# Optimization experiments

Hardware: AMD Instinct MI355X
Metric: run time of the kernel (lower is better)

The kernel has to match this reference:

```python
import jax, jax.numpy as jnp
import numpy as np

# Model dims (mamba_ssm defaults: expand=2, d_state=16, d_conv=4, dt_rank=ceil(d_model/16))
V, D_MODEL, N_LAYERS = 32000, 768, 2
D_INNER, D_STATE, D_CONV, DT_RANK = 1536, 16, 4, 48
BATCH, SEQ = 2, 2048


def setup_inputs() -> dict:
    key = jax.random.key(0)
    ks = jax.random.split(key, 10)

    def nrm(k, shape, s=0.02):
        return (jax.random.normal(k, shape) * s).astype(jnp.float32)

    x = jax.random.randint(ks[0], (BATCH, SEQ), 0, V)
    emb = nrm(ks[1], (V, D_MODEL))
    # per-layer Mamba params, stacked on leading layer axis
    W_in = nrm(ks[2], (N_LAYERS, 2 * D_INNER, D_MODEL))          # in_proj (no bias)
    conv_w = nrm(ks[3], (N_LAYERS, D_INNER, 1, D_CONV), 0.1)      # depthwise causal conv
    conv_b = jnp.zeros((N_LAYERS, D_INNER), jnp.float32)
    W_x = nrm(ks[4], (N_LAYERS, DT_RANK + 2 * D_STATE, D_INNER))  # x_proj (no bias)
    W_dt = nrm(ks[5], (N_LAYERS, D_INNER, DT_RANK), 0.05)         # dt_proj
    b_dt = jnp.full((N_LAYERS, D_INNER), -4.0, jnp.float32)       # softplus(-4) ~ small dt
    # A initialized as -exp(A_log) with A_log = log(1..d_state), per mamba_ssm
    A_log = jnp.log(jnp.broadcast_to(
        jnp.arange(1, D_STATE + 1, dtype=jnp.float32), (N_LAYERS, D_INNER, D_STATE)))
    D_skip = jnp.ones((N_LAYERS, D_INNER), jnp.float32)
    W_out = nrm(ks[6], (N_LAYERS, D_MODEL, D_INNER))              # out_proj (no bias)
    ln_g = jnp.ones((D_MODEL,), jnp.float32)
    ln_b = jnp.zeros((D_MODEL,), jnp.float32)
    head_w = nrm(ks[7], (V, D_MODEL))
    head_b = jnp.zeros((V,), jnp.float32)
    return dict(x=x, emb=emb, W_in=W_in, conv_w=conv_w, conv_b=conv_b, W_x=W_x,
                W_dt=W_dt, b_dt=b_dt, A_log=A_log, D_skip=D_skip, W_out=W_out,
                ln_g=ln_g, ln_b=ln_b, head_w=head_w, head_b=head_b)


def mamba_block(h, W_in, conv_w, conv_b, W_x, W_dt, b_dt, A_log, D_skip, W_out):
    # h: (B, L, D_MODEL)
    xz = jnp.einsum('bld,ed->ble', h, W_in)              # (B, L, 2*d_inner)
    u, z = jnp.split(xz, 2, axis=-1)
    # causal depthwise conv over time
    uc = jnp.transpose(u, (0, 2, 1))                     # (B, d_inner, L)
    uc = jax.lax.conv_general_dilated(
        uc, conv_w, window_strides=(1,), padding=[(D_CONV - 1, 0)],
        feature_group_count=D_INNER, dimension_numbers=('NCH', 'OIH', 'NCH'))
    u = jax.nn.silu(jnp.transpose(uc, (0, 2, 1)) + conv_b)
    # input-dependent dt, B, C
    x_dbl = jnp.einsum('bld,ed->ble', u, W_x)            # (B, L, dt_rank+2*d_state)
    dtl, Bm, Cm = jnp.split(x_dbl, [DT_RANK, DT_RANK + D_STATE], axis=-1)
    dt = jax.nn.softplus(jnp.einsum('blr,dr->bld', dtl, W_dt) + b_dt)  # (B, L, d_inner)
    A = -jnp.exp(A_log)                                  # (d_inner, d_state)

    def step(hst, inp):
        dt_t, u_t, B_t, C_t = inp                        # (B,d_inner),(B,d_inner),(B,d_state),(B,d_state)
        hst = jnp.exp(dt_t[..., None] * A) * hst + (dt_t * u_t)[..., None] * B_t[:, None, :]
        y_t = jnp.einsum('bds,bs->bd', hst, C_t)
        return hst, y_t

    h0 = jnp.zeros((u.shape[0], D_INNER, D_STATE), u.dtype)
    xs = (dt.transpose(1, 0, 2), u.transpose(1, 0, 2),
          Bm.transpose(1, 0, 2), Cm.transpose(1, 0, 2))
    _, ys = jax.lax.scan(step, h0, xs)                   # (L, B, d_inner)
    y = ys.transpose(1, 0, 2) + u * D_skip
    y = y * jax.nn.silu(z)
    return jnp.einsum('bli,oi->blo', y, W_out)           # back to (B, L, D_MODEL)


def reference(x, emb, W_in, conv_w, conv_b, W_x, W_dt, b_dt, A_log, D_skip,
              W_out, ln_g, ln_b, head_w, head_b):
    h = emb[x]                                           # (B, L, D_MODEL)
    for l in range(N_LAYERS):
        h = h + mamba_block(h, W_in[l], conv_w[l], conv_b[l], W_x[l], W_dt[l],
                            b_dt[l], A_log[l], D_skip[l], W_out[l])
    mu = jnp.mean(h, axis=-1, keepdims=True)
    var = jnp.mean((h - mu) ** 2, axis=-1, keepdims=True)
    hn = (h - mu) * jax.lax.rsqrt(var + 1e-5) * ln_g + ln_b
    return jnp.einsum('bld,vd->blv', hn, head_w) + head_b
```

## Files before the change

kernel.cpp:

```cpp
#include <hip/hip_runtime.h>
#include <hip/hip_bf16.h>
#include <stdint.h>

#define BL    4096
#define DM    768
#define DI    1536
#define DS    16
#define DCONV 4
#define DTR   48
#define NL    2
#define SEQL  2048
#define BATCH 2
#define VOC   32000
#define NCH   32
#define CT    64

typedef __bf16 bf16_t;
typedef __bf16 bf16x8 __attribute__((ext_vector_type(8)));
typedef __bf16 bf16x4 __attribute__((ext_vector_type(4)));
typedef float  f32x4  __attribute__((ext_vector_type(4)));

__device__ __forceinline__ float sigmoidf_(float x) { return 1.f / (1.f + __expf(-x)); }
__device__ __forceinline__ float softplus_(float x) {
  return (x > 20.f) ? x : log1pf(__expf(x));
}

__global__ __launch_bounds__(256) void k_embed(const int* __restrict__ x,
                                               const float* __restrict__ emb,
                                               float* __restrict__ h,
                                               bf16_t* __restrict__ hb) {
  int row = blockIdx.x;
  int tok = x[row];
  const float* e = emb + (size_t)tok * DM;
  float* hr = h + (size_t)row * DM;
  bf16_t* hbr = hb + (size_t)row * DM;
  for (int c = threadIdx.x; c < DM; c += 256) {
    float v = e[c];
    hr[c] = v;
    hbr[c] = (bf16_t)v;
  }
}

#define NV0 1179648L
#define NV1 589824L
#define NV2 6144000L
#define NS3 393216L
#define NS4 196608L
#define NVT (NV0 + NV1 + NV2)
#define NTOT (NVT + NS3 + NS4)

__global__ __launch_bounds__(256) void k_cvtw(const float* __restrict__ Win,
                                              const float* __restrict__ Wout,
                                              const float* __restrict__ Whead,
                                              const float* __restrict__ Wx,
                                              const float* __restrict__ Wdt,
                                              bf16_t* __restrict__ bin,
                                              bf16_t* __restrict__ bout,
                                              bf16_t* __restrict__ bhead,
                                              bf16_t* __restrict__ bx,
                                              bf16_t* __restrict__ bdt) {
  long i = (long)blockIdx.x * 256 + threadIdx.x;
  if (i >= NTOT) return;
  if (i < NVT) {
    const float* s; bf16_t* d; long j = i;
    if (i < NV0)            { s = Win;   d = bin; }
    else if (i < NV0 + NV1) { s = Wout;  d = bout;  j = i - NV0; }
    else                    { s = Whead; d = bhead; j = i - NV0 - NV1; }
    float4 v = ((const float4*)s)[j];
    bf16x4 o;
    o[0] = (bf16_t)v.x; o[1] = (bf16_t)v.y; o[2] = (bf16_t)v.z; o[3] = (bf16_t)v.w;
    ((bf16x4*)d)[j] = o;
  } else if (i < NVT + NS3) {
    long j = i - NVT;
    int l = (int)(j / (128 * 1536));
    int rr = (int)((j / 1536) % 128);
    int c = (int)(j % 1536);
    bx[j] = (bf16_t)(rr < 80 ? Wx[((long)l * 80 + rr) * 1536 + c] : 0.f);
  } else {
    long j = i - NVT - NS3;
    int l = (int)(j / (1536 * 64));
    int r = (int)((j / 64) % 1536);
    int c = (int)(j & 63);
    bdt[j] = (bf16_t)(c < DTR ? Wdt[((long)l * 1536 + r) * DTR + c] : 0.f);
  }
}

__global__ __launch_bounds__(256) void k_cvt_pad(const float* __restrict__ src,
                                                 bf16_t* __restrict__ dst,
                                                 int R, int C, int srcLd, int Cpad,
                                                 long total) {
  long i = (long)blockIdx.x * 256 + threadIdx.x;
  if (i >= total) return;
  int r = (int)(i / Cpad), c = (int)(i % Cpad);
  float v = (r < R && c < C) ? src[(size_t)r * srcLd + c] : 0.f;
  dst[i] = (bf16_t)v;
}

__global__ __launch_bounds__(256) void k_zero(float* __restrict__ p, long n4) {
  long i = (long)blockIdx.x * 256 + threadIdx.x;
  if (i < n4) ((float4*)p)[i] = (float4){0.f, 0.f, 0.f, 0.f};
}

__global__ __launch_bounds__(256) void k_conv(const float* __restrict__ xz,
                                              const float* __restrict__ cw,
                                              const float* __restrict__ cb,
                                              bf16_t* __restrict__ ucb, long total) {
  long i = (long)blockIdx.x * 256 + threadIdx.x;
  if (i >= total) return;
  int d = (int)(i % DI);
  long row = i / DI;
  int l = (int)(row % SEQL);
  const float* w = cw + (size_t)d * DCONV;
  float s = cb[d];
#pragma unroll
  for (int j = 0; j < DCONV; j++) {
    int lj = l - (DCONV - 1) + j;
    if (lj >= 0) s += xz[(row - (DCONV - 1) + j) * (2 * DI) + d] * w[j];
  }
  float v = s * sigmoidf_(s);
  ucb[i] = (bf16_t)v;
}

__global__ __launch_bounds__(256) void k_scan1(const float* __restrict__ dt,
                                               const bf16_t* __restrict__ uc,
                                               const float* __restrict__ xdbl,
                                               const float* __restrict__ A_log,
                                               float* __restrict__ cA,
                                               float* __restrict__ cB) {
  int gi = blockIdx.x * 256 + threadIdx.x;
  int s = gi & 15;
  int rest = gi >> 4;
  int d = rest % DI;
  int rest2 = rest / DI;
  int c = rest2 % NCH;
  int b = rest2 / NCH;
  float a = -__expf(A_log[d * DS + s]);
  long l0 = (long)c * CT;
  const float*  dtp = dt + ((long)b * SEQL + l0) * DI + d;
  const bf16_t* ucp = uc + ((long)b * SEQL + l0) * DI + d;
  const float*  Bp  = xdbl + ((long)b * SEQL + l0) * 80 + DTR + s;
  float S = 0.f, hh = 0.f;
#pragma unroll 4
  for (int l = 0; l < CT; l++) {
    float dtv = dtp[(long)l * DI];
    float uv  = (float)ucp[(long)l * DI];
    float Bv  = Bp[(long)l * 80];
    S += dtv;
    hh = __expf(dtv * a) * hh + (dtv * uv) * Bv;
  }
  cA[gi] = __expf(a * S);
  cB[gi] = hh;
}

__global__ __launch_bounds__(256) void k_scan2(const float* __restrict__ cA,
                                               const float* __restrict__ cB,
                                               float* __restrict__ hst) {
  int gj = blockIdx.x * 256 + threadIdx.x;
  int ds_ = gj & (DI * DS - 1);
  int b = gj / (DI * DS);
  float h = 0.f;
#pragma unroll
  for (int c = 0; c < NCH; c++) {
    long idx = ((long)(b * NCH + c) * DI * DS) + ds_;
    hst[idx] = h;
    h = cA[idx] * h + cB[idx];
  }
}

__global__ __launch_bounds__(256) void k_scan3g(const float* __restrict__ dt,
                                                const bf16_t* uc,
                                                const float* __restrict__ xdbl,
                                                const float* __restrict__ A_log,
                                                const float* __restrict__ hst,
                                                const float* __restrict__ xz,
                                                const float* __restrict__ Dsk,
                                                bf16_t* o) {
  int gi = blockIdx.x * 256 + threadIdx.x;
  int s = gi & 15;
  int rest = gi >> 4;
  int d = rest % DI;
  int rest2 = rest / DI;
  int c = rest2 % NCH;
  int b = rest2 / NCH;
  float a = -__expf(A_log[d * DS + s]);
  float dval = Dsk[d];
  long l0 = (long)c * CT;
  const float*  dtp = dt + ((long)b * SEQL + l0) * DI + d;
  const bf16_t* ucp = uc + ((long)b * SEQL + l0) * DI + d;
  const float*  Bp  = xdbl + ((long)b * SEQL + l0) * 80 + DTR + s;
  const float*  Cp  = Bp + DS;
  const float*  zp  = xz + ((long)b * SEQL + l0) * (2 * DI) + DI + d;
  bf16_t* yp = o + ((long)b * SEQL + l0) * DI + d;
  float h = hst[gi];
#pragma unroll 4
  for (int l = 0; l < CT; l++) {
    float dtv = dtp[(long)l * DI];
    float uv  = (float)ucp[(long)l * DI];
    float Bv  = Bp[(long)l * 80];
    float Cv  = Cp[(long)l * 80];
    h = __expf(dtv * a) * h + (dtv * uv) * Bv;
    float y = h * Cv;
    y += __shfl_xor(y, 1);
    y += __shfl_xor(y, 2);
    y += __shfl_xor(y, 4);
    y += __shfl_xor(y, 8);
    if (s == 0) {
      float z = zp[(long)l * 2 * DI];
      float yy = (y + uv * dval) * z * sigmoidf_(z);
      yp[(long)l * DI] = (bf16_t)yy;
    }
  }
}

__global__ __launch_bounds__(256) void k_ln(const float* __restrict__ h,
                                            const float* __restrict__ g,
                                            const float* __restrict__ bta,
                                            bf16_t* __restrict__ o) {
  __shared__ float sm[4];
  int row = blockIdx.x;
  int t = threadIdx.x;
  const float* hr = h + (long)row * DM;
  float v0 = hr[t], v1 = hr[t + 256], v2 = hr[t + 512];
  float s = v0 + v1 + v2;
#pragma unroll
  for (int off = 32; off > 0; off >>= 1) s += __shfl_down(s, off);
  if ((t & 63) == 0) sm[t >> 6] = s;
  __syncthreads();
  float mu = (sm[0] + sm[1] + sm[2] + sm[3]) * (1.f / DM);
  __syncthreads();
  float d0 = v0 - mu, d1 = v1 - mu, d2 = v2 - mu;
  float q = d0 * d0 + d1 * d1 + d2 * d2;
#pragma unroll
  for (int off = 32; off > 0; off >>= 1) q += __shfl_down(q, off);
  if ((t & 63) == 0) sm[t >> 6] = q;
  __syncthreads();
  float var = (sm[0] + sm[1] + sm[2] + sm[3]) * (1.f / DM);
  float rs = rsqrtf(var + 1e-5f);
  bf16_t* orow = o + (long)row * DM;
  orow[t]       = (bf16_t)(d0 * rs * g[t]       + bta[t]);
  orow[t + 256] = (bf16_t)(d1 * rs * g[t + 256] + bta[t + 256]);
  orow[t + 512] = (bf16_t)(d2 * rs * g[t + 512] + bta[t + 512]);
}

__device__ __forceinline__ void stage16(const bf16_t* gp, bf16_t* lp) {
  __builtin_amdgcn_global_load_lds(
      (const __attribute__((address_space(1))) uint32_t*)gp,
      (__attribute__((address_space(3))) uint32_t*)lp, 16, 0, 0);
}

#define WAITV8()  asm volatile("s_waitcnt vmcnt(8)" ::: "memory")
#define WAITV0()  asm volatile("s_waitcnt vmcnt(0)" ::: "memory")
#define BARRIER() do { __builtin_amdgcn_s_barrier();                            \
                       asm volatile("" ::: "memory"); } while (0)


#define GLD256(ab, j, ktt, pp) do {                                             \
    int idx_ = (j) * 512 + tid;                                                 \
    int r_ = idx_ >> 3; int c16_ = idx_ & 7;                                    \
    size_t col_ = (size_t)(ktt) * 64 + (size_t)((c16_ ^ (r_ & 7)) << 3);        \
    const bf16_t* gp_ = (ab) ? (Wp + ((size_t)(n0 + r_)) * K + col_)            \
                             : (Ap + ((size_t)(m0 + r_)) * K + col_);           \
    bf16_t* lp_ = lds + ((((pp) * 2 + (ab)) * 256 + r_) * 64) + c16_ * 8;       \
    stage16(gp_, lp_);                                                          \
  } while (0)

#define STAGE256(pp, ktt) do {                                                  \
    GLD256(0, 0, ktt, pp); GLD256(0, 1, ktt, pp);                               \
    GLD256(0, 2, ktt, pp); GLD256(0, 3, ktt, pp);                               \
    GLD256(1, 0, ktt, pp); GLD256(1, 1, ktt, pp);                               \
    GLD256(1, 2, ktt, pp); GLD256(1, 3, ktt, pp);                               \
  } while (0)

#define COMPUTE_KH(pp, kh) do {                                                 \
    const char* lb_ = (const char*)lds;                                         \
    bf16x8 bfr_[4];                                                             \
    _Pragma("unroll") for (int f = 0; f < 4; ++f) {                             \
      int row_ = wn * 64 + f * 16 + fr;                                         \
      int byte_ = (((pp) * 2 + 1) * 256 + row_) * 128 +                         \
                  (((kh) * 64 + kq * 16) ^ ((row_ & 7) << 4));                  \
      bfr_[f] = *(const bf16x8*)(lb_ + byte_);                                  \
    }                                                                           \
    _Pragma("unroll") for (int mg = 0; mg < 2; ++mg) {                          \
      bf16x8 afr_[4];                                                           \
      _Pragma("unroll") for (int f = 0; f < 4; ++f) {                           \
        int row_ = wm * 128 + mg * 64 + f * 16 + fr;                            \
        int byte_ = (((pp) * 2 + 0) * 256 + row_) * 128 +                       \
                    (((kh) * 64 + kq * 16) ^ ((row_ & 7) << 4));                \
        afr_[f] = *(const bf16x8*)(lb_ + byte_);                                \
      }                                                                         \
      __builtin_amdgcn_s_setprio(1);                                            \
      _Pragma("unroll") for (int fm = 0; fm < 4; ++fm)                          \
        _Pragma("unroll") for (int fn = 0; fn < 4; ++fn)                        \
          acc[mg * 4 + fm][fn] = __builtin_amdgcn_mfma_f32_16x16x32_bf16(       \
              afr_[fm], bfr_[fn], acc[mg * 4 + fm][fn], 0, 0, 0);               \
      __builtin_amdgcn_s_setprio(0);                                            \
    }                                                                           \
  } while (0)

template <int EPI>
__global__ __launch_bounds__(512, 2) void k_gemm256(const bf16_t* __restrict__ Ap,
                                                    const bf16_t* __restrict__ Wp,
                                                    float* __restrict__ C,
                                                    const float* __restrict__ bias,
                                                    int K, int ldc) {
  __shared__ bf16_t lds[2 * 2 * 256 * 64];
  const int tid = threadIdx.x;
  const int lane = tid & 63;
  const int wid = tid >> 6;
  const int wm = wid >> 2, wn = wid & 3;
  const int fr = lane & 15, kq = lane >> 4;

  const int cpx = gridDim.x >> 3;
  const int wg = ((int)blockIdx.x & 7) * cpx + ((int)blockIdx.x >> 3);
  const long m0 = (long)(wg & 15) * 256;
  const long n0 = (long)(wg >> 4) * 256;

  f32x4 acc[8][4];
#pragma unroll
  for (int i = 0; i < 8; i++)
#pragma unroll
    for (int j = 0; j < 4; j++) acc[i][j] = (f32x4){0.f, 0.f, 0.f, 0.f};

  STAGE256(0, 0);
  const int NT = K >> 6;
  for (int kt = 0; kt < NT; ++kt) {
    const int p = kt & 1;
    const bool pre = (kt + 1 < NT);
    if (pre) STAGE256(p ^ 1, kt + 1);
    if (pre) WAITV8(); else WAITV0();
    BARRIER();
    COMPUTE_KH(p, 0);
    COMPUTE_KH(p, 1);
    BARRIER();
  }

  {
    float* lf = (float*)(void*)lds;
    const int q = lane >> 4;
    const int cc = lane & 15;
    float4 bias4 = {0.f, 0.f, 0.f, 0.f};
    if (EPI == 1) bias4 = *(const float4*)&bias[n0 + lane * 4];
#pragma unroll
    for (int p = 0; p < 4; ++p) {
      __syncthreads();
      if (wm == (p >> 1)) {
        const int mgb = (p & 1) * 4;
#pragma unroll
        for (int m4 = 0; m4 < 4; ++m4)
#pragma unroll
          for (int n = 0; n < 4; ++n) {
            f32x4 v = acc[mgb + m4][n];
            float* dst = &lf[(m4 * 16 + q * 4) * 260 + wn * 64 + n * 16 + cc];
#pragma unroll
            for (int r = 0; r < 4; ++r) dst[r * 260] = v[r];
          }
      }
      __syncthreads();
      const long rowg0 = m0 + p * 64;
#pragma unroll
      for (int it = 0; it < 8; ++it) {
        int row_loc = wid * 8 + it;
        f32x4 v = *(const f32x4*)&lf[row_loc * 260 + lane * 4];
        float* gp = &C[(rowg0 + row_loc) * (long)ldc + n0 + lane * 4];
        if (EPI == 1) {
          v[0] += bias4.x; v[1] += bias4.y; v[2] += bias4.z; v[3] += bias4.w;
          __builtin_nontemporal_store(v, (f32x4*)gp);
        } else {
          *(f32x4*)gp = v;
        }
      }
    }
  }
}


#define GLD128(ab, j, ktt, pp) do {                                             \
    int idx_ = (j) * 256 + tid;                                                 \
    int r_ = idx_ >> 3; int c16_ = idx_ & 7;                                    \
    size_t col_ = kb + (size_t)(ktt) * 64 + (size_t)((c16_ ^ (r_ & 7)) << 3);   \
    const bf16_t* gp_ = (ab) ? (Wp + ((size_t)(n0 + r_)) * K + col_)            \
                             : (Ap + ((size_t)(m0 + r_)) * K + col_);           \
    bf16_t* lp_ = lds + ((((pp) * 2 + (ab)) * 128 + r_) * 64) + c16_ * 8;       \
    stage16(gp_, lp_);                                                          \
  } while (0)

#define STAGE128(pp, ktt) do {                                                  \
    GLD128(0, 0, ktt, pp); GLD128(0, 1, ktt, pp);                               \
    GLD128(0, 2, ktt, pp); GLD128(0, 3, ktt, pp);                               \
    GLD128(1, 0, ktt, pp); GLD128(1, 1, ktt, pp);                               \
    GLD128(1, 2, ktt, pp); GLD128(1, 3, ktt, pp);                               \
  } while (0)

#define COMPUTE128(pp, kh) do {                                                 \
    const char* lb_ = (const char*)lds;                                         \
    bf16x8 af_[4], bv_[4];                                                      \
    _Pragma("unroll") for (int f = 0; f < 4; ++f) {                             \
      int row_ = wn * 64 + f * 16 + fr;                                         \
      int byte_ = (((pp) * 2 + 1) * 128 + row_) * 128 +                         \
                  (((kh) * 64 + kq * 16) ^ ((row_ & 7) << 4));                  \
      bv_[f] = *(const bf16x8*)(lb_ + byte_);                                   \
    }                                                                           \
    _Pragma("unroll") for (int f = 0; f < 4; ++f) {                             \
      int row_ = wm * 64 + f * 16 + fr;                                         \
      int byte_ = (((pp) * 2 + 0) * 128 + row_) * 128 +                         \
                  (((kh) * 64 + kq * 16) ^ ((row_ & 7) << 4));                  \
      af_[f] = *(const bf16x8*)(lb_ + byte_);                                   \
    }                                                                           \
    __builtin_amdgcn_s_setprio(1);                                              \
    _Pragma("unroll") for (int fm = 0; fm < 4; ++fm)                            \
      _Pragma("unroll") for (int fn = 0; fn < 4; ++fn)                          \
        acc[fm][fn] = __builtin_amdgcn_mfma_f32_16x16x32_bf16(                  \
            af_[fm], bv_[fn], acc[fm][fn], 0, 0, 0);                            \
    __builtin_amdgcn_s_setprio(0);                                              \
  } while (0)

template <int EPI>
__global__ __launch_bounds__(256, 2) void k_gemm128(const bf16_t* __restrict__ Ap,
                                                    const bf16_t* __restrict__ Wp,
                                                    float* __restrict__ C,
                                                    const float* __restrict__ bias,
                                                    bf16_t* __restrict__ side,
                                                    int K, int Ksl, int ldc) {
  __shared__ bf16_t lds[2 * 2 * 128 * 64];
  const int tid = threadIdx.x;
  const int lane = tid & 63;
  const int wv = tid >> 6;
  const int wm = wv >> 1, wn = wv & 1;
  const int fr = lane & 15, kq = lane >> 4;
  const size_t kb = (size_t)blockIdx.y * Ksl;

  const int cpx = gridDim.x >> 3;
  const int wg = ((int)blockIdx.x & 7) * cpx + ((int)blockIdx.x >> 3);
  const long m0 = (long)(wg & 31) * 128;
  const long n0 = (long)(wg >> 5) * 128;

  f32x4 acc[4][4];
#pragma unroll
  for (int i = 0; i < 4; i++)
#pragma unroll
    for (int j = 0; j < 4; j++) acc[i][j] = (f32x4){0.f, 0.f, 0.f, 0.f};

  STAGE128(0, 0);
  const int NT = Ksl >> 6;
  for (int kt = 0; kt < NT; ++kt) {
    const int p = kt & 1;
    const bool pre = (kt + 1 < NT);
    if (pre) STAGE128(p ^ 1, kt + 1);
    if (pre) WAITV8(); else WAITV0();
    BARRIER();
    COMPUTE128(p, 0);
    COMPUTE128(p, 1);
    BARRIER();
  }

  if (EPI == 6) {
    const int r4 = (lane >> 4) * 4;
    const int cc = lane & 15;
#pragma unroll
    for (int fm = 0; fm < 4; fm++) {
      long rowb = m0 + wm * 64 + fm * 16 + r4;
#pragma unroll
      for (int fn = 0; fn < 4; fn++) {
        long col = n0 + wn * 64 + fn * 16 + cc;
        if (col < 80) {
#pragma unroll
          for (int r = 0; r < 4; r++)
            atomicAdd(&C[(rowb + r) * (long)ldc + col], acc[fm][fn][r]);
        }
      }
    }
    return;
  }

  {
    float* lf = (float*)(void*)lds;
    const int q = lane >> 4;
    const int cc = lane & 15;
    const int colt = (tid & 31) * 4;
    float4 bias4 = {0.f, 0.f, 0.f, 0.f};
    if (EPI == 3) bias4 = *(const float4*)&bias[n0 + colt];
#pragma unroll
    for (int p = 0; p < 4; ++p) {
      __syncthreads();
      if (wm == (p >> 1)) {
#pragma unroll
        for (int fl = 0; fl < 2; ++fl) {
          int fm = (p & 1) * 2 + fl;
#pragma unroll
          for (int fn = 0; fn < 4; ++fn) {
            f32x4 v = acc[fm][fn];
            float* dst = &lf[(fl * 16 + q * 4) * 132 + wn * 64 + fn * 16 + cc];
#pragma unroll
            for (int r = 0; r < 4; ++r) dst[r * 132] = v[r];
          }
        }
      }
      __syncthreads();
      const long rowg0 = m0 + p * 32;
#pragma unroll
      for (int it = 0; it < 4; ++it) {
        int rl = it * 8 + (tid >> 5);
        f32x4 v = *(const f32x4*)&lf[rl * 132 + colt];
        long row = rowg0 + rl;
        long cg = n0 + colt;
        float* gp = &C[row * (long)ldc + cg];
        if (EPI == 3) {
          v[0] = softplus_(v[0] + bias4.x);
          v[1] = softplus_(v[1] + bias4.y);
          v[2] = softplus_(v[2] + bias4.z);
          v[3] = softplus_(v[3] + bias4.w);
          *(f32x4*)gp = v;
        } else {
          f32x4 c0 = *(const f32x4*)gp;
          v[0] += c0[0]; v[1] += c0[1]; v[2] += c0[2]; v[3] += c0[3];
          *(f32x4*)gp = v;
          bf16x4 s4;
          s4[0] = (bf16_t)v[0]; s4[1] = (bf16_t)v[1];
          s4[2] = (bf16_t)v[2]; s4[3] = (bf16_t)v[3];
          *(bf16x4*)&side[row * (long)ldc + cg] = s4;
        }
      }
    }
  }
}

static inline int cdiv_l(long a, long b) { return (int)((a + b - 1) / b); }

extern "C" void kernel_launch(void* const* d_in, const int* in_sizes, int n_in,
                              void* d_out, int out_size, void* d_ws, size_t ws_size,
                              hipStream_t stream) {
  (void)in_sizes; (void)n_in; (void)out_size; (void)ws_size;
  const int*   x      = (const int*)  d_in[0];
  const float* emb    = (const float*)d_in[1];
  const float* W_in   = (const float*)d_in[2];
  const float* conv_w = (const float*)d_in[3];
  const float* conv_b = (const float*)d_in[4];
  const float* W_x    = (const float*)d_in[5];
  const float* W_dt   = (const float*)d_in[6];
  const float* b_dt   = (const float*)d_in[7];
  const float* A_log  = (const float*)d_in[8];
  const float* D_skip = (const float*)d_in[9];
  const float* W_out  = (const float*)d_in[10];
  const float* ln_g   = (const float*)d_in[11];
  const float* ln_b   = (const float*)d_in[12];
  const float* head_w = (const float*)d_in[13];
  const float* head_b = (const float*)d_in[14];
  float* out = (float*)d_out;

  bf16_t* abuf   = (bf16_t*)d_ws;
  bf16_t* hbf    = abuf   + (size_t)BL * DI;
  bf16_t* dtl    = hbf    + (size_t)BL * DM;
  bf16_t* wb_in  = dtl    + (size_t)BL * 64;
  bf16_t* wb_out = wb_in  + (size_t)2 * 3072 * 768;
  bf16_t* wb_hd  = wb_out + (size_t)2 * 768 * 1536;
  bf16_t* wb_x   = wb_hd  + (size_t)VOC * DM;
  bf16_t* wb_dt  = wb_x   + (size_t)2 * 128 * 1536;

  float* xz   = out;
  float* xdbl = xz   + (size_t)BL * 2 * DI;
  float* dtb  = xdbl + (size_t)BL * 80;
  float* h    = dtb  + (size_t)BL * DI;
  float* cA   = h    + (size_t)BL * DM;
  float* cB   = cA   + (size_t)BATCH * NCH * DI * DS;
  float* hst  = cB   + (size_t)BATCH * NCH * DI * DS;

  const int scan_blocks = BATCH * NCH * DI * DS / 256;
  const int st_blocks   = BATCH * DI * DS / 256;

  k_cvtw<<<cdiv_l(NTOT, 256), 256, 0, stream>>>(W_in, W_out, head_w, W_x, W_dt,
                                                wb_in, wb_out, wb_hd, wb_x, wb_dt);
  k_embed<<<BL, 256, 0, stream>>>(x, emb, h, hbf);

  for (int l = 0; l < NL; ++l) {
    k_gemm256<0><<<(BL / 256) * (2 * DI / 256), 512, 0, stream>>>(
        hbf, wb_in + (size_t)l * 3072 * 768, xz, nullptr, DM, 2 * DI);
    k_conv<<<cdiv_l((long)BL * DI, 256), 256, 0, stream>>>(
        xz, conv_w + (size_t)l * DI * DCONV, conv_b + (size_t)l * DI,
        abuf, (long)BL * DI);
    k_zero<<<cdiv_l((long)BL * 80 / 4, 256), 256, 0, stream>>>(xdbl, (long)BL * 80 / 4);
    k_gemm128<6><<<dim3(32, 4), 256, 0, stream>>>(
        abuf, wb_x + (size_t)l * 128 * 1536, xdbl, nullptr, nullptr,
        DI, DI / 4, 80);
    k_cvt_pad<<<cdiv_l((long)BL * 64, 256), 256, 0, stream>>>(
        xdbl, dtl, BL, DTR, 80, 64, (long)BL * 64);
    k_gemm128<3><<<(BL / 128) * (DI / 128), 256, 0, stream>>>(
        dtl, wb_dt + (size_t)l * 1536 * 64, dtb, b_dt + (size_t)l * DI, nullptr,
        64, 64, DI);
    k_scan1<<<scan_blocks, 256, 0, stream>>>(dtb, abuf, xdbl,
                                             A_log + (size_t)l * DI * DS, cA, cB);
    k_scan2<<<st_blocks, 256, 0, stream>>>(cA, cB, hst);
    k_scan3g<<<scan_blocks, 256, 0, stream>>>(dtb, abuf, xdbl,
                                              A_log + (size_t)l * DI * DS, hst,
                                              xz, D_skip + (size_t)l * DI, abuf);
    k_gemm128<5><<<(BL / 128) * (DM / 128), 256, 0, stream>>>(
        abuf, wb_out + (size_t)l * 768 * 1536, h, nullptr, hbf, DI, DI, DM);
  }

  k_ln<<<BL, 256, 0, stream>>>(h, ln_g, ln_b, abuf);
  k_gemm256<1><<<(BL / 256) * (VOC / 256), 512, 0, stream>>>(
      abuf, wb_hd, out, head_b, DM, VOC);
}
```

Baseline: 988.4 us.

## Interleave GEMM global-to-LDS prefetch with MFMA phases and fuse zeroing into conv

The 256x256 GEMM main loop now splits next-tile global-to-LDS staging into four pairs of loads. Each pair is issued between LDS fragment reads and an MFMA group, with barriers around each MFMA group, so memory traffic is spread across the compute phases instead of issued all at once. Separately, the k_zero launch is removed and the xdbl zeroing is folded into the conv kernel, saving one launch per layer. The extra barriers per k-step could add synchronisation cost. The wait now only covers the first two loads of the next tile, so correctness relies on the later per-tile waits draining the interleaved loads in time.

New measurement: 994.8 us. Within noise of the previous version (+0.6%).

```diff
diff --git a/kernel.cpp b/kernel.cpp
--- a/kernel.cpp
+++ b/kernel.cpp
@@ -96,16 +96,13 @@
   dst[i] = (bf16_t)v;
 }
 
-__global__ __launch_bounds__(256) void k_zero(float* __restrict__ p, long n4) {
-  long i = (long)blockIdx.x * 256 + threadIdx.x;
-  if (i < n4) ((float4*)p)[i] = (float4){0.f, 0.f, 0.f, 0.f};
-}
-
 __global__ __launch_bounds__(256) void k_conv(const float* __restrict__ xz,
                                               const float* __restrict__ cw,
                                               const float* __restrict__ cb,
-                                              bf16_t* __restrict__ ucb, long total) {
+                                              bf16_t* __restrict__ ucb, long total,
+                                              float* __restrict__ zbuf, long nz4) {
   long i = (long)blockIdx.x * 256 + threadIdx.x;
+  if (i < nz4) ((float4*)zbuf)[i] = (float4){0.f, 0.f, 0.f, 0.f};
   if (i >= total) return;
   int d = (int)(i % DI);
   long row = i / DI;
@@ -249,6 +246,7 @@
 }
 
 #define WAITV8()  asm volatile("s_waitcnt vmcnt(8)" ::: "memory")
+#define WAITV2()  asm volatile("s_waitcnt vmcnt(2)" ::: "memory")
 #define WAITV0()  asm volatile("s_waitcnt vmcnt(0)" ::: "memory")
 #define BARRIER() do { __builtin_amdgcn_s_barrier();                            \
                        asm volatile("" ::: "memory"); } while (0)
@@ -271,30 +269,29 @@
     GLD256(1, 2, ktt, pp); GLD256(1, 3, ktt, pp);                               \
   } while (0)
 
-#define COMPUTE_KH(pp, kh) do {                                                 \
-    const char* lb_ = (const char*)lds;                                         \
-    bf16x8 bfr_[4];                                                             \
+#define READ_B(pp, kh)                                                          \
     _Pragma("unroll") for (int f = 0; f < 4; ++f) {                             \
       int row_ = wn * 64 + f * 16 + fr;                                         \
       int byte_ = (((pp) * 2 + 1) * 256 + row_) * 128 +                         \
                   (((kh) * 64 + kq * 16) ^ ((row_ & 7) << 4));                  \
-      bfr_[f] = *(const bf16x8*)(lb_ + byte_);                                  \
-    }                                                                           \
-    _Pragma("unroll") for (int mg = 0; mg < 2; ++mg) {                          \
-      bf16x8 afr_[4];                                                           \
-      _Pragma("unroll") for (int f = 0; f < 4; ++f) {                           \
-        int row_ = wm * 128 + mg * 64 + f * 16 + fr;                            \
-        int byte_ = (((pp) * 2 + 0) * 256 + row_) * 128 +                       \
-                    (((kh) * 64 + kq * 16) ^ ((row_ & 7) << 4));                \
-        afr_[f] = *(const bf16x8*)(lb_ + byte_);                                \
-      }                                                                         \
-      __builtin_amdgcn_s_setprio(1);                                            \
-      _Pragma("unroll") for (int fm = 0; fm < 4; ++fm)                          \
-        _Pragma("unroll") for (int fn = 0; fn < 4; ++fn)                        \
-          acc[mg * 4 + fm][fn] = __builtin_amdgcn_mfma_f32_16x16x32_bf16(       \
-              afr_[fm], bfr_[fn], acc[mg * 4 + fm][fn], 0, 0, 0);               \
-      __builtin_amdgcn_s_setprio(0);                                            \
-    }                                                                           \
+      bfr[f] = *(const bf16x8*)(lb + byte_);                                    \
+    }
+
+#define READ_A(pp, kh, mg)                                                      \
+    _Pragma("unroll") for (int f = 0; f < 4; ++f) {                             \
+      int row_ = wm * 128 + (mg) * 64 + f * 16 + fr;                            \
+      int byte_ = (((pp) * 2 + 0) * 256 + row_) * 128 +                         \
+                  (((kh) * 64 + kq * 16) ^ ((row_ & 7) << 4));                  \
+      afr[f] = *(const bf16x8*)(lb + byte_);                                    \
+    }
+
+#define MFMA16(mg) do {                                                         \
+    __builtin_amdgcn_s_setprio(1);                                              \
+    _Pragma("unroll") for (int fm = 0; fm < 4; ++fm)                            \
+      _Pragma("unroll") for (int fn = 0; fn < 4; ++fn)                          \
+        acc[(mg) * 4 + fm][fn] = __builtin_amdgcn_mfma_f32_16x16x32_bf16(       \
+            afr[fm], bfr[fn], acc[(mg) * 4 + fm][fn], 0, 0, 0);                 \
+    __builtin_amdgcn_s_setprio(0);                                              \
   } while (0)
 
 template <int EPI>
@@ -326,12 +323,24 @@
   for (int kt = 0; kt < NT; ++kt) {
     const int p = kt & 1;
     const bool pre = (kt + 1 < NT);
-    if (pre) STAGE256(p ^ 1, kt + 1);
-    if (pre) WAITV8(); else WAITV0();
+    if (pre) { GLD256(0, 0, kt + 1, p ^ 1); GLD256(0, 1, kt + 1, p ^ 1); }
+    if (pre) WAITV2(); else WAITV0();
     BARRIER();
-    COMPUTE_KH(p, 0);
-    COMPUTE_KH(p, 1);
-    BARRIER();
+    {
+      const char* lb = (const char*)lds;
+      bf16x8 bfr[4], afr[4];
+      READ_B(p, 0); READ_A(p, 0, 0);
+      if (pre) { GLD256(1, 0, kt + 1, p ^ 1); GLD256(1, 1, kt + 1, p ^ 1); }
+      BARRIER(); MFMA16(0); BARRIER();
+      READ_A(p, 0, 1);
+      if (pre) { GLD256(0, 2, kt + 1, p ^ 1); GLD256(0, 3, kt + 1, p ^ 1); }
+      BARRIER(); MFMA16(1); BARRIER();
+      READ_B(p, 1); READ_A(p, 1, 0);
+      if (pre) { GLD256(1, 2, kt + 1, p ^ 1); GLD256(1, 3, kt + 1, p ^ 1); }
+      BARRIER(); MFMA16(0); BARRIER();
+      READ_A(p, 1, 1);
+      BARRIER(); MFMA16(1); BARRIER();
+    }
   }
 
   {
@@ -576,8 +585,7 @@
         hbf, wb_in + (size_t)l * 3072 * 768, xz, nullptr, DM, 2 * DI);
     k_conv<<<cdiv_l((long)BL * DI, 256), 256, 0, stream>>>(
         xz, conv_w + (size_t)l * DI * DCONV, conv_b + (size_t)l * DI,
-        abuf, (long)BL * DI);
-    k_zero<<<cdiv_l((long)BL * 80 / 4, 256), 256, 0, stream>>>(xdbl, (long)BL * 80 / 4);
+        abuf, (long)BL * DI, xdbl, (long)BL * 80 / 4);
     k_gemm128<6><<<dim3(32, 4), 256, 0, stream>>>(
         abuf, wb_x + (size_t)l * 128 * 1536, xdbl, nullptr, nullptr,
         DI, DI / 4, 80);
```

## Replace split-K atomics with partial buffers and store dt as bf16

Applied to the files above, without the earlier changes.

The x_proj split-K GEMM now writes four partial tiles to a scratch buffer instead of atomically adding into a zeroed xdbl. A new reduce kernel sums the partials and also emits the padded bf16 dt-low-rank input, so the separate zero and convert-pad kernels are dropped. The pad columns are zeroed once inside the embed kernel. The dt_proj epilogue writes softplus output as bf16, which halves the dt traffic read by both scan kernels at the cost of reduced dt precision.

Result: no change. 974.7 us (-1.4%).

```diff
diff --git a/kernel.cpp b/kernel.cpp
--- a/kernel.cpp
+++ b/kernel.cpp
@@ -28,8 +28,13 @@
 __global__ __launch_bounds__(256) void k_embed(const int* __restrict__ x,
                                                const float* __restrict__ emb,
                                                float* __restrict__ h,
-                                               bf16_t* __restrict__ hb) {
+                                               bf16_t* __restrict__ hb,
+                                               bf16_t* __restrict__ dtl) {
   int row = blockIdx.x;
+  if (row < 256) {
+    int r = row * 16 + (threadIdx.x >> 4);
+    dtl[r * 64 + 48 + (threadIdx.x & 15)] = (bf16_t)0.f;
+  }
   int tok = x[row];
   const float* e = emb + (size_t)tok * DM;
   float* hr = h + (size_t)row * DM;
@@ -85,22 +90,6 @@
   }
 }
 
-__global__ __launch_bounds__(256) void k_cvt_pad(const float* __restrict__ src,
-                                                 bf16_t* __restrict__ dst,
-                                                 int R, int C, int srcLd, int Cpad,
-                                                 long total) {
-  long i = (long)blockIdx.x * 256 + threadIdx.x;
-  if (i >= total) return;
-  int r = (int)(i / Cpad), c = (int)(i % Cpad);
-  float v = (r < R && c < C) ? src[(size_t)r * srcLd + c] : 0.f;
-  dst[i] = (bf16_t)v;
-}
-
-__global__ __launch_bounds__(256) void k_zero(float* __restrict__ p, long n4) {
-  long i = (long)blockIdx.x * 256 + threadIdx.x;
-  if (i < n4) ((float4*)p)[i] = (float4){0.f, 0.f, 0.f, 0.f};
-}
-
 __global__ __launch_bounds__(256) void k_conv(const float* __restrict__ xz,
                                               const float* __restrict__ cw,
                                               const float* __restrict__ cb,
@@ -121,7 +110,18 @@
   ucb[i] = (bf16_t)v;
 }
 
-__global__ __launch_bounds__(256) void k_scan1(const float* __restrict__ dt,
+__global__ __launch_bounds__(256) void k_xfin(const float* __restrict__ xp,
+                                              float* __restrict__ xdbl,
+                                              bf16_t* __restrict__ dtl) {
+  long i = (long)blockIdx.x * 256 + threadIdx.x;
+  if (i >= (long)BL * 80) return;
+  float s = xp[i] + xp[i + (long)BL * 80] + xp[i + 2L * BL * 80] + xp[i + 3L * BL * 80];
+  xdbl[i] = s;
+  int row = (int)(i / 80), col = (int)(i % 80);
+  if (col < DTR) dtl[(long)row * 64 + col] = (bf16_t)s;
+}
+
+__global__ __launch_bounds__(256) void k_scan1(const bf16_t* __restrict__ dt,
                                                const bf16_t* __restrict__ uc,
                                                const float* __restrict__ xdbl,
                                                const float* __restrict__ A_log,
@@ -136,13 +136,13 @@
   int b = rest2 / NCH;
   float a = -__expf(A_log[d * DS + s]);
   long l0 = (long)c * CT;
-  const float*  dtp = dt + ((long)b * SEQL + l0) * DI + d;
+  const bf16_t* dtp = dt + ((long)b * SEQL + l0) * DI + d;
   const bf16_t* ucp = uc + ((long)b * SEQL + l0) * DI + d;
   const float*  Bp  = xdbl + ((long)b * SEQL + l0) * 80 + DTR + s;
   float S = 0.f, hh = 0.f;
 #pragma unroll 4
   for (int l = 0; l < CT; l++) {
-    float dtv = dtp[(long)l * DI];
+    float dtv = (float)dtp[(long)l * DI];
     float uv  = (float)ucp[(long)l * DI];
     float Bv  = Bp[(long)l * 80];
     S += dtv;
@@ -167,7 +167,7 @@
   }
 }
 
-__global__ __launch_bounds__(256) void k_scan3g(const float* __restrict__ dt,
+__global__ __launch_bounds__(256) void k_scan3g(const bf16_t* __restrict__ dt,
                                                 const bf16_t* uc,
                                                 const float* __restrict__ xdbl,
                                                 const float* __restrict__ A_log,
@@ -185,7 +185,7 @@
   float a = -__expf(A_log[d * DS + s]);
   float dval = Dsk[d];
   long l0 = (long)c * CT;
-  const float*  dtp = dt + ((long)b * SEQL + l0) * DI + d;
+  const bf16_t* dtp = dt + ((long)b * SEQL + l0) * DI + d;
   const bf16_t* ucp = uc + ((long)b * SEQL + l0) * DI + d;
   const float*  Bp  = xdbl + ((long)b * SEQL + l0) * 80 + DTR + s;
   const float*  Cp  = Bp + DS;
@@ -194,7 +194,7 @@
   float h = hst[gi];
 #pragma unroll 4
   for (int l = 0; l < CT; l++) {
-    float dtv = dtp[(long)l * DI];
+    float dtv = (float)dtp[(long)l * DI];
     float uv  = (float)ucp[(long)l * DI];
     float Bv  = Bp[(long)l * 80];
     float Cv  = Cp[(long)l * 80];
@@ -252,7 +252,6 @@
 #define WAITV0()  asm volatile("s_waitcnt vmcnt(0)" ::: "memory")
 #define BARRIER() do { __builtin_amdgcn_s_barrier();                            \
                        asm volatile("" ::: "memory"); } while (0)
-
 
 #define GLD256(ab, j, ktt, pp) do {                                             \
     int idx_ = (j) * 512 + tid;                                                 \
@@ -373,7 +372,6 @@
   }
 }
 
-
 #define GLD128(ab, j, ktt, pp) do {                                             \
     int idx_ = (j) * 256 + tid;                                                 \
     int r_ = idx_ >> 3; int c16_ = idx_ & 7;                                    \
@@ -453,7 +451,8 @@
     BARRIER();
   }
 
-  if (EPI == 6) {
+  if (EPI == 7) {
+    float* Cs = C + (size_t)blockIdx.y * (size_t)BL * 80;
     const int r4 = (lane >> 4) * 4;
     const int cc = lane & 15;
 #pragma unroll
@@ -465,7 +464,7 @@
         if (col < 80) {
 #pragma unroll
           for (int r = 0; r < 4; r++)
-            atomicAdd(&C[(rowb + r) * (long)ldc + col], acc[fm][fn][r]);
+            Cs[(rowb + r) * 80 + col] = acc[fm][fn][r];
         }
       }
     }
@@ -478,7 +477,7 @@
     const int cc = lane & 15;
     const int colt = (tid & 31) * 4;
     float4 bias4 = {0.f, 0.f, 0.f, 0.f};
-    if (EPI == 3) bias4 = *(const float4*)&bias[n0 + colt];
+    if (EPI == 4) bias4 = *(const float4*)&bias[n0 + colt];
 #pragma unroll
     for (int p = 0; p < 4; ++p) {
       __syncthreads();
@@ -503,14 +502,15 @@
         f32x4 v = *(const f32x4*)&lf[rl * 132 + colt];
         long row = rowg0 + rl;
         long cg = n0 + colt;
-        float* gp = &C[row * (long)ldc + cg];
-        if (EPI == 3) {
-          v[0] = softplus_(v[0] + bias4.x);
-          v[1] = softplus_(v[1] + bias4.y);
-          v[2] = softplus_(v[2] + bias4.z);
-          v[3] = softplus_(v[3] + bias4.w);
-          *(f32x4*)gp = v;
+        if (EPI == 4) {
+          bf16x4 s4;
+          s4[0] = (bf16_t)softplus_(v[0] + bias4.x);
+          s4[1] = (bf16_t)softplus_(v[1] + bias4.y);
+          s4[2] = (bf16_t)softplus_(v[2] + bias4.z);
+          s4[3] = (bf16_t)softplus_(v[3] + bias4.w);
+          *(bf16x4*)&side[row * (long)ldc + cg] = s4;
         } else {
+          float* gp = &C[row * (long)ldc + cg];
           f32x4 c0 = *(const f32x4*)gp;
           v[0] += c0[0]; v[1] += c0[1]; v[2] += c0[2]; v[3] += c0[3];
           *(f32x4*)gp = v;
@@ -556,20 +556,22 @@
   bf16_t* wb_x   = wb_hd  + (size_t)VOC * DM;
   bf16_t* wb_dt  = wb_x   + (size_t)2 * 128 * 1536;
 
-  float* xz   = out;
-  float* xdbl = xz   + (size_t)BL * 2 * DI;
-  float* dtb  = xdbl + (size_t)BL * 80;
-  float* h    = dtb  + (size_t)BL * DI;
-  float* cA   = h    + (size_t)BL * DM;
-  float* cB   = cA   + (size_t)BATCH * NCH * DI * DS;
-  float* hst  = cB   + (size_t)BATCH * NCH * DI * DS;
+  float*  xz    = out;
+  float*  xdbl  = xz    + (size_t)BL * 2 * DI;
+  float*  dtb_f = xdbl  + (size_t)BL * 80;
+  bf16_t* dtbb  = (bf16_t*)dtb_f;
+  float*  h     = dtb_f + (size_t)BL * DI;
+  float*  cA    = h     + (size_t)BL * DM;
+  float*  cB    = cA    + (size_t)BATCH * NCH * DI * DS;
+  float*  hst   = cB    + (size_t)BATCH * NCH * DI * DS;
+  float*  xpart = hst   + (size_t)BATCH * DI * DS;
 
   const int scan_blocks = BATCH * NCH * DI * DS / 256;
   const int st_blocks   = BATCH * DI * DS / 256;
 
   k_cvtw<<<cdiv_l(NTOT, 256), 256, 0, stream>>>(W_in, W_out, head_w, W_x, W_dt,
                                                 wb_in, wb_out, wb_hd, wb_x, wb_dt);
-  k_embed<<<BL, 256, 0, stream>>>(x, emb, h, hbf);
+  k_embed<<<BL, 256, 0, stream>>>(x, emb, h, hbf, dtl);
 
   for (int l = 0; l < NL; ++l) {
     k_gemm256<0><<<(BL / 256) * (2 * DI / 256), 512, 0, stream>>>(
@@ -577,19 +579,17 @@
     k_conv<<<cdiv_l((long)BL * DI, 256), 256, 0, stream>>>(
         xz, conv_w + (size_t)l * DI * DCONV, conv_b + (size_t)l * DI,
         abuf, (long)BL * DI);
-    k_zero<<<cdiv_l((long)BL * 80 / 4, 256), 256, 0, stream>>>(xdbl, (long)BL * 80 / 4);
-    k_gemm128<6><<<dim3(32, 4), 256, 0, stream>>>(
-        abuf, wb_x + (size_t)l * 128 * 1536, xdbl, nullptr, nullptr,
+    k_gemm128<7><<<dim3(32, 4), 256, 0, stream>>>(
+        abuf, wb_x + (size_t)l * 128 * 1536, xpart, nullptr, nullptr,
         DI, DI / 4, 80);
-    k_cvt_pad<<<cdiv_l((long)BL * 64, 256), 256, 0, stream>>>(
-        xdbl, dtl, BL, DTR, 80, 64, (long)BL * 64);
-    k_gemm128<3><<<(BL / 128) * (DI / 128), 256, 0, stream>>>(
-        dtl, wb_dt + (size_t)l * 1536 * 64, dtb, b_dt + (size_t)l * DI, nullptr,
+    k_xfin<<<cdiv_l((long)BL * 80, 256), 256, 0, stream>>>(xpart, xdbl, dtl);
+    k_gemm128<4><<<(BL / 128) * (DI / 128), 256, 0, stream>>>(
+        dtl, wb_dt + (size_t)l * 1536 * 64, nullptr, b_dt + (size_t)l * DI, dtbb,
         64, 64, DI);
-    k_scan1<<<scan_blocks, 256, 0, stream>>>(dtb, abuf, xdbl,
+    k_scan1<<<scan_blocks, 256, 0, stream>>>(dtbb, abuf, xdbl,
                                              A_log + (size_t)l * DI * DS, cA, cB);
     k_scan2<<<st_blocks, 256, 0, stream>>>(cA, cB, hst);
-    k_scan3g<<<scan_blocks, 256, 0, stream>>>(dtb, abuf, xdbl,
+    k_scan3g<<<scan_blocks, 256, 0, stream>>>(dtbb, abuf, xdbl,
                                               A_log + (size_t)l * DI * DS, hst,
                                               xz, D_skip + (size_t)l * DI, abuf);
     k_gemm128<5><<<(BL / 128) * (DM / 128), 256, 0, stream>>>(
```
